# Kernel tuning notes

Measured on AMD Instinct MI355X. Metric: run time of the kernel, lower is better.

Reference implementation:

```python
import jax, jax.numpy as jnp
import numpy as np

DEPTH = 13                 # tree depth -> N = 2**DEPTH - 1 reaches (heap layout, outlet = node 0)
N = 2 ** DEPTH - 1         # 8191 reaches
T = 2048                   # timesteps


def setup_inputs() -> dict:
    key = jax.random.key(0)
    ks = jax.random.split(key, 8)
    u = lambda k, shape, lo, hi: jax.random.uniform(k, shape, minval=lo, maxval=hi, dtype=jnp.float32)
    return {
        "lateral_inflows": u(ks[0], (T, N), 0.0, 2.0),     # m^3/s lateral inflow per reach
        "manning_n":       u(ks[1], (N,), 0.025, 0.06),    # Manning roughness
        "lengths":         u(ks[2], (N,), 1000.0, 5000.0), # reach length [m]
        "slopes":          u(ks[3], (N,), 1e-4, 1e-2),     # bed slope (>= 1e-4 as in source)
        "width_coefs":     u(ks[4], (N,), 3.0, 10.0),      # w = wc * Q**we  (power-law geometry)
        "width_exps":      u(ks[5], (N,), 0.4, 0.6),
        "depth_coefs":     u(ks[6], (N,), 0.2, 0.5),       # h = dc * Q**de
        "depth_exps":      u(ks[7], (N,), 0.3, 0.45),
        "dt": 3600,                                        # routing timestep [s]
    }


def _mc_outflow(I_new, I_old, O_old, n, L, S, wc, we, dc, de, dt):
    """Variable-parameter Muskingum-Cunge update for one vector of reaches."""
    Qr = jnp.maximum(0.5 * (I_new + O_old), 1e-3)          # reference discharge
    h = dc * Qr ** de                                       # hydraulic depth
    w = wc * Qr ** we                                       # top width
    v = h ** (2.0 / 3.0) * jnp.sqrt(S) / n                  # Manning velocity
    c = jnp.maximum((5.0 / 3.0) * v, 1e-3)                  # kinematic celerity
    K = L / c                                               # travel time
    X = jnp.clip(0.5 * (1.0 - Qr / (w * S * c * L)), 0.0, 0.5)
    den = 2.0 * K * (1.0 - X) + dt
    C1 = (dt - 2.0 * K * X) / den
    C2 = (dt + 2.0 * K * X) / den
    C3 = (2.0 * K * (1.0 - X) - dt) / den
    return jnp.maximum(C1 * I_new + C2 * I_old + C3 * O_old, 0.0)


def reference(lateral_inflows, manning_n, lengths, slopes, width_coefs, width_exps,
              depth_coefs, depth_exps, dt):
    dtf = jnp.float32(dt)
    Np = lateral_inflows.shape[1]
    params = (manning_n, lengths, slopes, width_coefs, width_exps, depth_coefs, depth_exps)

    def step(carry, lat_t):
        I_old, O_old = carry                                # [N] prev inflow / outflow
        Q = jnp.zeros(Np, dtype=lat_t.dtype)                # new outflows this timestep
        I_all = jnp.zeros(Np, dtype=lat_t.dtype)
        # process levels leaves -> root (reverse topological order over the DAG)
        for l in range(DEPTH - 1, -1, -1):
            s, e = 2 ** l - 1, 2 ** (l + 1) - 1             # nodes of level l
            if l == DEPTH - 1:
                up = jnp.float32(0.0)                        # headwater reaches
            else:
                cs, ce = 2 ** (l + 1) - 1, 2 ** (l + 2) - 1  # children = level l+1
                up = Q[cs:ce:2] + Q[cs + 1:ce:2]             # sum of 2 upstream discharges
            I_new = lat_t[s:e] + up
            O_new = _mc_outflow(I_new, I_old[s:e], O_old[s:e],
                                *(p[s:e] for p in params), dtf)
            Q = Q.at[s:e].set(O_new)
            I_all = I_all.at[s:e].set(I_new)
        return (I_all, Q), Q[0]                              # outlet = root (index 0)

    init = (jnp.zeros(Np, jnp.float32), jnp.zeros(Np, jnp.float32))
    _, outlet_Q = jax.lax.scan(step, init, lateral_inflows)
    return outlet_Q                                          # [T]
```

## Files before the change

kernel.cpp:

```cpp
#include <hip/hip_runtime.h>


#define NN 8191
#define TT 2048
#define FBATCH 32
#define NBLK 39
#define BTHREADS 256

#define FLAGS_FOFF 16773120ull
#define REQ_BYTES  67106816ull
#define FLAG_STRIDE 16

#if __has_builtin(__builtin_amdgcn_exp2f)
__device__ __forceinline__ float fexp2(float x) { return __builtin_amdgcn_exp2f(x); }
#else
__device__ __forceinline__ float fexp2(float x) { return exp2f(x); }
#endif
#if __has_builtin(__builtin_amdgcn_logf)
__device__ __forceinline__ float flog2(float x) { return __builtin_amdgcn_logf(x); }
#else
__device__ __forceinline__ float flog2(float x) { return log2f(x); }
#endif
#if __has_builtin(__builtin_amdgcn_rcpf)
__device__ __forceinline__ float frcp(float x) { return __builtin_amdgcn_rcpf(x); }
#else
__device__ __forceinline__ float frcp(float x) { return 1.0f / x; }
#endif

__constant__ int g_level[NBLK] = {
    12,12,12,12,12,12,12,12,12,12,12,12,12,12,12,12,
    11,11,11,11,11,11,11,11,
    10,10,10,10,
    9,9,
    8,7,6,5,4,3,2,1,0};
__constant__ int g_cnt[NBLK] = {
    256,256,256,256,256,256,256,256,256,256,256,256,256,256,256,256,
    256,256,256,256,256,256,256,256,
    256,256,256,256,
    256,256,
    256,128,64,32,16,8,4,2,1};
__constant__ int g_first[13] = {38,37,36,35,34,33,32,31,30,28,24,16,0};
__constant__ unsigned long long g_off[13] = {
    16773120ull, 16769024ull, 16760832ull, 16744448ull, 16711680ull,
    16646144ull, 16515072ull, 16252928ull, 15728640ull, 14680064ull,
    12582912ull, 8388608ull, 0ull};

__device__ __forceinline__ void waitflags(const unsigned int* fa, const unsigned int* fb,
                                          unsigned int target)
{
    while (true) {
        unsigned int a = __hip_atomic_load(fa, __ATOMIC_RELAXED, __HIP_MEMORY_SCOPE_AGENT);
        unsigned int b = fb ? __hip_atomic_load(fb, __ATOMIC_RELAXED, __HIP_MEMORY_SCOPE_AGENT)
                            : a;
        if (a >= target && b >= target) break;
        __builtin_amdgcn_s_sleep(1);
    }
    __builtin_amdgcn_sched_barrier(0);
    asm volatile("" ::: "memory");
}

__global__ void zero_flags(unsigned int* flags)
{
    for (int i = threadIdx.x; i < NBLK * 4 * FLAG_STRIDE; i += 256) flags[i] = 0;
}

__global__ __launch_bounds__(BTHREADS, 1)
void pipe_kernel(const float* __restrict__ lat,
                 const float* __restrict__ nman,
                 const float* __restrict__ len,
                 const float* __restrict__ slp,
                 const float* __restrict__ wcf,
                 const float* __restrict__ wex,
                 const float* __restrict__ dcf,
                 const float* __restrict__ dex,
                 const int*   __restrict__ dtp,
                 float*       __restrict__ out,
                 float*       __restrict__ ws)
{
    const int bid = blockIdx.x;
    const int tid = threadIdx.x;
    const int lvl = g_level[bid];
    const int cnt = g_cnt[bid];
    const int W   = tid >> 6;
    const int wn  = cnt - W * 64;
    if (wn <= 0) return;

    const bool active = (tid < cnt);
    const int B = bid - g_first[lvl];
    const int m = B * 256 + (active ? tid : 0);
    const int node = ((1 << lvl) - 1) + m;
    const int wbase = B * 256 + W * 64;

    unsigned int* flags = (unsigned int*)(ws + FLAGS_FOFF);
    unsigned int* myflag = flags + ((size_t)bid * 4 + W) * FLAG_STRIDE;

    const bool haschild = (lvl < 12);
    const unsigned int* fa = nullptr;
    const unsigned int* fb = nullptr;
    if (haschild) {
        const int Fp = g_first[lvl + 1];
        const int nw = wn < 64 ? wn : 64;
        const int p0 = (2 * wbase) >> 6;
        const int p1 = (2 * wbase + 2 * nw - 1) >> 6;
        fa = flags + ((size_t)(Fp + (p0 >> 2)) * 4 + (p0 & 3)) * FLAG_STRIDE;
        fb = (p1 != p0)
           ? flags + ((size_t)(Fp + (p1 >> 2)) * 4 + (p1 & 3)) * FLAG_STRIDE
           : nullptr;
    }

    const int myW = 1 << lvl;
    const int childW = 1 << (lvl + 1);
    float* myBuf = ws + g_off[lvl];
    const unsigned long long* childBuf =
        haschild ? (const unsigned long long*)(ws + g_off[lvl + 1]) : nullptr;

    const float dtf = (float)dtp[0];

    float em, tkc, ex, k1;
    float Iold = 0.0f, Oold = 0.0f;
    {
        float n = nman[node], L = len[node], S = slp[node];
        float wc = wcf[node], we = wex[node], dc = dcf[node], de = dex[node];
        float dc23 = fexp2(0.6666667f * flog2(dc));
        float cc = 1.6666667f * dc23 * sqrtf(S) * frcp(n);
        float e23 = 0.6666667f * de;
        em  = -e23;
        tkc = 2.0f * L * frcp(cc);
        ex  = 1.0f - we - e23;
        k1  = 0.5f * frcp(S * L * wc * cc);
    }

    float la[FBATCH];
    unsigned long long cv[FBATCH];

    for (int t0 = 0; t0 < TT; t0 += FBATCH) {
        if (active) {
#pragma unroll
            for (int k = 0; k < FBATCH; ++k) {
                const float* lp = lat + (size_t)(t0 + k) * NN + node;
                asm volatile("global_load_dword %0, %1, off"
                             : "=v"(la[k]) : "v"(lp));
            }
        }

        if (haschild) waitflags(fa, fb, (unsigned int)(t0 + FBATCH));

        if (haschild && active) {
#pragma unroll
            for (int k = 0; k < FBATCH; ++k) {
                const unsigned long long* cp =
                    childBuf + (((size_t)(t0 + k) * childW) >> 1) + m;
                asm volatile("global_load_dwordx2 %0, %1, off sc0 sc1"
                             : "=v"(cv[k]) : "v"(cp));
            }
        }

        asm volatile("s_waitcnt vmcnt(0)" ::: "memory");
        __builtin_amdgcn_sched_barrier(0);

        if (active) {
#pragma unroll
            for (int k = 0; k < FBATCH; ++k) {
                float ch = 0.0f;
                if (haschild) {
                    float c0 = __uint_as_float((unsigned int)(cv[k] & 0xffffffffull));
                    float c1 = __uint_as_float((unsigned int)(cv[k] >> 32));
                    ch = c0 + c1;
                }
                float Inew = la[k] + ch;
                float Qr = fmaxf(0.5f * (Inew + Oold), 1e-3f);
                float lg = flog2(Qr);
                float twoK = tkc * fexp2(em * lg);
                float X = fmaxf(0.5f - k1 * fexp2(ex * lg), 0.0f);
                float A = twoK * X;
                float Bv = twoK - A;
                float r = frcp(Bv + dtf);
                float num = dtf * (Inew + Iold - Oold) + A * (Iold - Inew) + Bv * Oold;
                float O = fmaxf(num * r, 0.0f);
                Iold = Inew; Oold = O;
                if (lvl > 0)
                    __hip_atomic_store(myBuf + (size_t)(t0 + k) * myW + m, O,
                                       __ATOMIC_RELAXED, __HIP_MEMORY_SCOPE_AGENT);
                else
                    out[t0 + k] = O;
            }
        }

        if (lvl > 0) {
            asm volatile("s_waitcnt vmcnt(0)" ::: "memory");
            if ((tid & 63) == 0)
                __hip_atomic_store(myflag, (unsigned int)(t0 + FBATCH),
                                   __ATOMIC_RELAXED, __HIP_MEMORY_SCOPE_AGENT);
        }
    }
}

#define NTHREADS 1024
__device__ __forceinline__ float mc_update_fb(float Inew, float Iold, float Oold,
                                              float em, float tkc, float ex, float k1,
                                              float dtf)
{
    float Qr = fmaxf(0.5f * (Inew + Oold), 1e-3f);
    float lg = flog2(Qr);
    float twoK = tkc * fexp2(em * lg);
    float X = fmaxf(0.5f - k1 * fexp2(ex * lg), 0.0f);
    float A = twoK * X;
    float B = twoK - A;
    float r = frcp(B + dtf);
    float C1 = (dtf - A) * r;
    float C2 = (dtf + A) * r;
    float C3 = (B - dtf) * r;
    return fmaxf(C1 * Inew + C2 * Iold + C3 * Oold, 0.0f);
}

__global__ __launch_bounds__(NTHREADS)
void route_kernel(const float* __restrict__ lat,
                  const float* __restrict__ nman,
                  const float* __restrict__ len,
                  const float* __restrict__ slp,
                  const float* __restrict__ wcf,
                  const float* __restrict__ wex,
                  const float* __restrict__ dcf,
                  const float* __restrict__ dex,
                  const int*   __restrict__ dtp,
                  float*       __restrict__ out)
{
    __shared__ float Osh[NN];
    const int tid = threadIdx.x;
    const float dtf = (float)dtp[0];

    int nodes[8];
    nodes[0] = 4095 + tid;
    nodes[1] = 5119 + tid;
    nodes[2] = 6143 + tid;
    nodes[3] = 7167 + tid;
    nodes[4] = 2047 + tid;
    nodes[5] = 3071 + tid;
    nodes[6] = 1023 + tid;
    nodes[7] = (tid < 1023) ? tid : 0;

    float em[8], tkc[8], ex[8], k1[8];
    float Ireg[8], Oreg[8];
#pragma unroll
    for (int k = 0; k < 8; ++k) {
        int i = nodes[k];
        float n = nman[i], L = len[i], S = slp[i];
        float wc = wcf[i], we = wex[i], dc = dcf[i], de = dex[i];
        float dc23 = fexp2(0.6666667f * flog2(dc));
        float cc = 1.6666667f * dc23 * sqrtf(S) * frcp(n);
        float e23 = 0.6666667f * de;
        em[k]  = -e23;
        tkc[k] = 2.0f * L * frcp(cc);
        ex[k]  = 1.0f - we - e23;
        k1[k]  = 0.5f * frcp(S * L * wc * cc);
        Ireg[k] = 0.0f; Oreg[k] = 0.0f;
    }
    for (int i = tid; i < NN; i += NTHREADS) Osh[i] = 0.0f;
    __syncthreads();

    for (int t = 0; t < TT; ++t) {
        const float* __restrict__ latt = lat + (size_t)t * NN;
#pragma unroll
        for (int k = 0; k < 4; ++k) {
            int i = nodes[k];
            float Inew = latt[i];
            float O = mc_update_fb(Inew, Ireg[k], Oreg[k], em[k], tkc[k], ex[k], k1[k], dtf);
            Ireg[k] = Inew; Oreg[k] = O; Osh[i] = O;
        }
        __syncthreads();
#pragma unroll
        for (int k = 4; k < 6; ++k) {
            int i = nodes[k];
            float Inew = latt[i] + Osh[2 * i + 1] + Osh[2 * i + 2];
            float O = mc_update_fb(Inew, Ireg[k], Oreg[k], em[k], tkc[k], ex[k], k1[k], dtf);
            Ireg[k] = Inew; Oreg[k] = O; Osh[i] = O;
        }
        __syncthreads();
        {
            int i = nodes[6];
            float Inew = latt[i] + Osh[2 * i + 1] + Osh[2 * i + 2];
            float O = mc_update_fb(Inew, Ireg[6], Oreg[6], em[6], tkc[6], ex[6], k1[6], dtf);
            Ireg[6] = Inew; Oreg[6] = O; Osh[i] = O;
        }
        __syncthreads();
        for (int l = 9; l >= 0; --l) {
            int s = (1 << l) - 1;
            int e = (1 << (l + 1)) - 1;
            if (tid >= s && tid < e) {
                int i = tid;
                float Inew = latt[i] + Osh[2 * i + 1] + Osh[2 * i + 2];
                float O = mc_update_fb(Inew, Ireg[7], Oreg[7], em[7], tkc[7], ex[7], k1[7], dtf);
                Ireg[7] = Inew; Oreg[7] = O; Osh[i] = O;
            }
            __syncthreads();
        }
        if (tid == 0) out[t] = Oreg[7];
    }
}

extern "C" void kernel_launch(void* const* d_in, const int* in_sizes, int n_in,
                              void* d_out, int out_size, void* d_ws, size_t ws_size,
                              hipStream_t stream) {
    const float* lat  = (const float*)d_in[0];
    const float* nman = (const float*)d_in[1];
    const float* len  = (const float*)d_in[2];
    const float* slp  = (const float*)d_in[3];
    const float* wcf  = (const float*)d_in[4];
    const float* wex  = (const float*)d_in[5];
    const float* dcf  = (const float*)d_in[6];
    const float* dex  = (const float*)d_in[7];
    const int*   dtp  = (const int*)d_in[8];
    float* out = (float*)d_out;

    if (ws_size >= REQ_BYTES) {
        float* ws = (float*)d_ws;
        unsigned int* flags = (unsigned int*)(ws + FLAGS_FOFF);
        zero_flags<<<dim3(1), dim3(256), 0, stream>>>(flags);
        pipe_kernel<<<dim3(NBLK), dim3(BTHREADS), 0, stream>>>(
            lat, nman, len, slp, wcf, wex, dcf, dex, dtp, out, ws);
    } else {
        route_kernel<<<dim3(1), dim3(NTHREADS), 0, stream>>>(
            lat, nman, len, slp, wcf, wex, dcf, dex, dtp, out);
    }
}
```

Before: 404.0 us.

## Break serial time recurrence latency with predicted-Q transcendental precompute and Taylor correction

The per-timestep Muskingum-Cunge update is restructured so the expensive log2/exp2/rcp chain is computed two steps ahead from a predicted reference discharge, obtained by reusing the previous step's coefficients. The true step then corrects the precomputed powers with a 4th-order Taylor polynomial in the relative error d, clamped to ±0.4, and refines the reciprocal with two Newton iterations. This is meant to take the transcendental latency off the serial dependency chain across timesteps. In exchange it adds extra FMAs and register pressure, and it risks accuracy loss when the prediction error is large and the clamp engages.

```diff
diff --git a/kernel.cpp b/kernel.cpp
--- a/kernel.cpp
+++ b/kernel.cpp
@@ -116,7 +116,7 @@
 
     const float dtf = (float)dtp[0];
 
-    float em, tkc, ex, k1;
+    float em, eme, tkc, p1c, p2c, c2e, c3e, c4e, c2m, c3m, c4m;
     float Iold = 0.0f, Oold = 0.0f;
     {
         float n = nman[node], L = len[node], S = slp[node];
@@ -125,13 +125,35 @@
         float cc = 1.6666667f * dc23 * sqrtf(S) * frcp(n);
         float e23 = 0.6666667f * de;
         em  = -e23;
+        eme = 1.0f - we - 2.0f * e23;
         tkc = 2.0f * L * frcp(cc);
-        ex  = 1.0f - we - e23;
-        k1  = 0.5f * frcp(S * L * wc * cc);
+        float k1 = 0.5f * frcp(S * L * wc * cc);
+        p1c = 0.5f * tkc;
+        p2c = k1 * tkc;
+        c2e = 0.5f * em * (em - 1.0f);
+        c3e = c2e * (em - 2.0f) * 0.33333333f;
+        c4e = c3e * (em - 3.0f) * 0.25f;
+        c2m = 0.5f * eme * (eme - 1.0f);
+        c3m = c2m * (eme - 2.0f) * 0.33333333f;
+        c4m = c3m * (eme - 3.0f) * 0.25f;
     }
 
     float la[FBATCH];
     unsigned long long cv[FBATCH];
+    float Inw[FBATCH];
+
+    float pR[3], pE1[3], pE12[3], pr[3];
+    float twoK_s = 0.0f, A_s = 0.0f, r_s = 0.0f;
+
+#define PACKCALC(S, QH)                                                        \
+    {                                                                          \
+        float lgh_ = flog2(QH);                                                \
+        pE1[S]  = fexp2(em * lgh_);                                            \
+        pE12[S] = fexp2(eme * lgh_);                                           \
+        pR[S]   = frcp(QH);                                                    \
+        float Ah_ = fmaxf(fmaf(-p2c, pE12[S], p1c * pE1[S]), 0.0f);            \
+        pr[S]   = frcp(fmaf(tkc, pE1[S], dtf) - Ah_);                          \
+    }
 
     for (int t0 = 0; t0 < TT; t0 += FBATCH) {
         if (active) {
@@ -167,17 +189,54 @@
                     float c1 = __uint_as_float((unsigned int)(cv[k] >> 32));
                     ch = c0 + c1;
                 }
-                float Inew = la[k] + ch;
-                float Qr = fmaxf(0.5f * (Inew + Oold), 1e-3f);
-                float lg = flog2(Qr);
-                float twoK = tkc * fexp2(em * lg);
-                float X = fmaxf(0.5f - k1 * fexp2(ex * lg), 0.0f);
-                float A = twoK * X;
-                float Bv = twoK - A;
-                float r = frcp(Bv + dtf);
-                float num = dtf * (Inew + Iold - Oold) + A * (Iold - Inew) + Bv * Oold;
-                float O = fmaxf(num * r, 0.0f);
-                Iold = Inew; Oold = O;
+                Inw[k] = la[k] + ch;
+            }
+
+            {
+                float Qh0 = fmaxf(0.5f * (Inw[0] + Oold), 1e-3f);
+                PACKCALC(0, Qh0);
+                twoK_s = tkc * pE1[0];
+                A_s = fmaxf(fmaf(-p2c, pE12[0], p1c * pE1[0]), 0.0f);
+                r_s = pr[0];
+                float s1h = (Inw[0] + Iold) - Oold;
+                float s2h = fmaf(-2.0f, Inw[0], s1h);
+                float Oh = fmaxf(fmaf(A_s, s2h, fmaf(twoK_s, Oold, dtf * s1h)) * r_s, 0.0f);
+                float Qh1 = fmaxf(0.5f * (Inw[1] + Oh), 1e-3f);
+                PACKCALC(1, Qh1);
+            }
+
+#pragma unroll
+            for (int k = 0; k < FBATCH; ++k) {
+                float s1 = (Inw[k] + Iold) - Oold;
+                float s2 = fmaf(-2.0f, Inw[k], s1);
+
+                if (k < FBATCH - 2) {
+                    float Oh0 = fmaxf(fmaf(A_s, s2, fmaf(twoK_s, Oold, dtf * s1)) * r_s, 0.0f);
+                    float sh1 = (Inw[k + 1] + Inw[k]) - Oh0;
+                    float sh2 = fmaf(-2.0f, Inw[k + 1], sh1);
+                    float Oh1 = fmaxf(fmaf(A_s, sh2, fmaf(twoK_s, Oh0, dtf * sh1)) * r_s, 0.0f);
+                    float Qh = fmaxf(0.5f * (Inw[k + 2] + Oh1), 1e-3f);
+                    PACKCALC((k + 2) % 3, Qh);
+                }
+
+                const int c = k % 3;
+                float Qr = fmaxf(0.5f * (Inw[k] + Oold), 1e-3f);
+                float d = fmaf(Qr, pR[c], -1.0f);
+                d = fminf(fmaxf(d, -0.4f), 0.4f);
+                float f1 = fmaf(fmaf(fmaf(fmaf(c4e, d, c3e), d, c2e), d, em), d, 1.0f);
+                float f2 = fmaf(fmaf(fmaf(fmaf(c4m, d, c3m), d, c2m), d, eme), d, 1.0f);
+                float E1 = pE1[c] * f1;
+                float E12 = pE12[c] * f2;
+                float twoK = tkc * E1;
+                float A = fmaxf(fmaf(-p2c, E12, p1c * E1), 0.0f);
+                float den = (twoK + dtf) - A;
+                float rr = pr[c];
+                rr = rr * fmaf(-den, rr, 2.0f);
+                rr = rr * fmaf(-den, rr, 2.0f);
+                float num = fmaf(A, s2, fmaf(twoK, Oold, dtf * s1));
+                float O = fmaxf(num * rr, 0.0f);
+                twoK_s = twoK; A_s = A; r_s = rr;
+                Iold = Inw[k]; Oold = O;
                 if (lvl > 0)
                     __hip_atomic_store(myBuf + (size_t)(t0 + k) * myW + m, O,
                                        __ATOMIC_RELAXED, __HIP_MEMORY_SCOPE_AGENT);
@@ -193,6 +252,7 @@
                                    __ATOMIC_RELAXED, __HIP_MEMORY_SCOPE_AGENT);
         }
     }
+#undef PACKCALC
 }
 
 #define NTHREADS 1024
```

Measured after the change: 578.4 us. 43.2% more time.
